# Kernel optimization log

Hardware: AMD Instinct MI355X
Metric: run time of the kernel (lower is better)

## Reference

```python
import jax, jax.numpy as jnp
import numpy as np

D_MODEL = 1024
N_STATE = 1024


def setup_inputs() -> dict:
    key = jax.random.key(0)
    k_x, k_A, k_Bw, k_Bb, k_Cw, k_Cb = jax.random.split(key, 6)
    x = jax.random.normal(k_x, (8, 2048, D_MODEL), dtype=jnp.float32)
    log_A = jax.random.normal(k_A, (N_STATE,), dtype=jnp.float32) * 0.1 - 1.0
    # nn.Linear default init: U(-1/sqrt(fan_in), 1/sqrt(fan_in)); weight is [out, in]
    bnd_B = 1.0 / np.sqrt(D_MODEL)
    B_w = jax.random.uniform(k_Bw, (N_STATE, D_MODEL), minval=-bnd_B, maxval=bnd_B, dtype=jnp.float32)
    B_b = jax.random.uniform(k_Bb, (N_STATE,), minval=-bnd_B, maxval=bnd_B, dtype=jnp.float32)
    bnd_C = 1.0 / np.sqrt(N_STATE)
    C_w = jax.random.uniform(k_Cw, (D_MODEL, N_STATE), minval=-bnd_C, maxval=bnd_C, dtype=jnp.float32)
    C_b = jax.random.uniform(k_Cb, (D_MODEL,), minval=-bnd_C, maxval=bnd_C, dtype=jnp.float32)
    return {"x": x, "log_A": log_A, "B_w": B_w, "B_b": B_b, "C_w": C_w, "C_b": C_b}


def _ssm_scan(A, B_x):
    """Diagonal linear recurrence h_t = A * h_{t-1} + B_x_t (h_0 prior = 0).

    Implemented as a parallel associative scan over the time axis.
    A: [N], B_x: [B, T, N] -> h: [B, T, N]
    """
    a = jnp.broadcast_to(A, B_x.shape)  # [B, T, N]

    def combine(c1, c2):
        a1, b1 = c1
        a2, b2 = c2
        return (a1 * a2, a2 * b1 + b2)

    _, h = jax.lax.associative_scan(combine, (a, B_x), axis=1)
    return h


def reference(x, log_A, B_w, B_b, C_w, C_b):
    A = jax.nn.sigmoid(log_A)                                  # [N]
    B_x = jnp.einsum('btd,nd->btn', x, B_w) + B_b              # [B, T, N]
    h = _ssm_scan(A, B_x)                                      # [B, T, N]
    y = jnp.einsum('btn,dn->btd', h, C_w) + C_b                # [B, T, D]
    return y
```

## Files before the change

kernel.cpp:

```cpp
#include <hip/hip_runtime.h>
#include <hip/hip_bf16.h>
#include <cstdint>
#include <cstddef>


typedef __attribute__((ext_vector_type(8))) short short8;
typedef __attribute__((ext_vector_type(4))) float f32x4;

#define AS_GLOBAL(p) ((const __attribute__((address_space(1))) void*)(p))
#define AS_LDS(p)    ((__attribute__((address_space(3))) void*)(p))

__device__ __forceinline__ unsigned short f2bf(float f) {
    union { float f; unsigned u; } v; v.f = f;
    return (unsigned short)((v.u + 0x7FFFu + ((v.u >> 16) & 1u)) >> 16);
}
__device__ __forceinline__ float bf2f(unsigned short u) {
    union { float f; unsigned u; } v; v.u = ((unsigned)u) << 16;
    return v.f;
}

__global__ void cvt_all(const float4* __restrict__ x, const float4* __restrict__ bw,
                        const float4* __restrict__ cw, ushort4* __restrict__ xo,
                        ushort4* __restrict__ bo, ushort4* __restrict__ co) {
    const int NX = (16384 * 1024) / 4;
    const int NW = (1024 * 1024) / 4;
    int i = blockIdx.x * blockDim.x + threadIdx.x;
    int stride = gridDim.x * blockDim.x;
    for (; i < NX + 2 * NW; i += stride) {
        const float4* s; ushort4* d; int j;
        if (i < NX)           { s = x;  d = xo; j = i; }
        else if (i < NX + NW) { s = bw; d = bo; j = i - NX; }
        else                  { s = cw; d = co; j = i - NX - NW; }
        float4 v = s[j];
        d[j] = make_ushort4(f2bf(v.x), f2bf(v.y), f2bf(v.z), f2bf(v.w));
    }
}

__global__ __launch_bounds__(256, 2)
void gemm1_scan_fused(const unsigned short* __restrict__ A,
                      const unsigned short* __restrict__ B,
                      const float* __restrict__ bias,
                      const float* __restrict__ logA,
                      unsigned short* __restrict__ H,
                      int M, int N, int K)
{
    constexpr int BK = 32, SXS = 130;
    __shared__ __align__(16) unsigned short smem[20800];
    unsigned short* As = smem;
    unsigned short* Bs = smem + 5120;
    unsigned short* Sx = smem;

    const int tid  = threadIdx.x;
    const int lane = tid & 63;
    const int wave = tid >> 6;
    const int wr   = wave >> 1;
    const int wm   = wr * 64;
    const int wn   = (wave & 1) * 64;
    const int q    = lane >> 4;
    const int l16  = lane & 15;
    const int m0   = blockIdx.x * 128;
    const int n0   = blockIdx.y * 128;

    const int rsub = lane >> 2;
    const int c8   = (lane & 3) * 8;

    f32x4 acc[4][4] = {};
    f32x4 accw[4]   = {};

    for (int k0 = 0; k0 < K; k0 += BK) {
        #pragma unroll
        for (int p = 0; p < 2; ++p) {
            const int rowbase = p * 64 + wave * 16;
            int gra = m0 - 32 + rowbase + rsub; if (gra < 0) gra = 0;
            const unsigned short* ga = A + (size_t)gra * K + k0 + c8;
            const unsigned short* gb = B + (size_t)(n0 + rowbase + rsub) * K + k0 + c8;
            __builtin_amdgcn_global_load_lds(AS_GLOBAL(ga), AS_LDS(&As[rowbase * BK]), 16, 0, 0);
            __builtin_amdgcn_global_load_lds(AS_GLOBAL(gb), AS_LDS(&Bs[rowbase * BK]), 16, 0, 0);
        }
        if (tid < 128) {
            const int rowbase = 128 + wave * 16;
            const unsigned short* ga = A + (size_t)(m0 - 32 + rowbase + rsub) * K + k0 + c8;
            __builtin_amdgcn_global_load_lds(AS_GLOBAL(ga), AS_LDS(&As[rowbase * BK]), 16, 0, 0);
        }
        __syncthreads();

        short8 a[4], aw, b[4];
        #pragma unroll
        for (int i = 0; i < 4; ++i)
            a[i] = *reinterpret_cast<const short8*>(&As[(32 + wm + i * 16 + l16) * BK + q * 8]);
        aw = *reinterpret_cast<const short8*>(&As[(wr * 16 + l16) * BK + q * 8]);
        #pragma unroll
        for (int j = 0; j < 4; ++j)
            b[j] = *reinterpret_cast<const short8*>(&Bs[(wn + j * 16 + l16) * BK + q * 8]);

        #pragma unroll
        for (int i = 0; i < 4; ++i)
            #pragma unroll
            for (int j = 0; j < 4; ++j)
                acc[i][j] = __builtin_amdgcn_mfma_f32_16x16x32_bf16(a[i], b[j], acc[i][j], 0, 0, 0);
        #pragma unroll
        for (int j = 0; j < 4; ++j)
            accw[j] = __builtin_amdgcn_mfma_f32_16x16x32_bf16(aw, b[j], accw[j], 0, 0, 0);
        __syncthreads();
    }

    float bcol[4];
    #pragma unroll
    for (int j = 0; j < 4; ++j)
        bcol[j] = bias[n0 + wn + j * 16 + l16];

    #pragma unroll
    for (int j = 0; j < 4; ++j) {
        #pragma unroll
        for (int r = 0; r < 4; ++r)
            Sx[(wr * 16 + q * 4 + r) * SXS + wn + j * 16 + l16] = f2bf(accw[j][r] + bcol[j]);
        #pragma unroll
        for (int i = 0; i < 4; ++i)
            #pragma unroll
            for (int r = 0; r < 4; ++r)
                Sx[(32 + wm + i * 16 + q * 4 + r) * SXS + wn + j * 16 + l16] = f2bf(acc[i][j][r] + bcol[j]);
    }
    __syncthreads();

    const int col  = tid & 127;
    const int half = tid >> 7;
    const int n    = n0 + col;
    const float Aa = 1.0f / (1.0f + __expf(-logA[n]));
    const bool chunk0 = (blockIdx.x & 15) == 0;

    float h = 0.0f;
    const int rw = half ? 64 : 0;
    if (!(half == 0 && chunk0)) {
        #pragma unroll
        for (int r = 0; r < 32; ++r)
            h = fmaf(Aa, h, bf2f(Sx[(rw + r) * SXS + col]));
    }
    const int rs = half ? 96 : 32;
    size_t o = (size_t)(m0 + (half ? 64 : 0)) * 1024 + n;
    #pragma unroll 8
    for (int r = 0; r < 64; ++r) {
        h = fmaf(Aa, h, bf2f(Sx[(rs + r) * SXS + col]));
        H[o] = f2bf(h);
        o += 1024;
    }
}

__global__ __launch_bounds__(512, 2)
void gemm2_8ph(const unsigned short* __restrict__ A,
               const unsigned short* __restrict__ B,
               const float* __restrict__ bias,
               float* __restrict__ C,
               int M, int N, int K)
{
    constexpr int BK  = 64;
    constexpr int NKT = 16;
    __shared__ __align__(16) unsigned short As[2][256 * BK];
    __shared__ __align__(16) unsigned short Bs[2][256 * BK];

    const int tid  = threadIdx.x;
    const int lane = tid & 63;
    const int wave = tid >> 6;
    const int wm   = (wave >> 2) * 128;
    const int wn   = (wave & 3) * 64;
    const int q    = lane >> 4;
    const int l16  = lane & 15;
    const int swx  = (l16 & 7) << 4;
    const int m0   = blockIdx.x * 256;
    const int n0   = blockIdx.y * 256;

    int dOff[4], sRow[4], sCol[4];
    #pragma unroll
    for (int p = 0; p < 4; ++p) {
        const int d = tid * 16 + p * 8192;
        const int l = d ^ (((d >> 7) & 7) << 4);
        dOff[p] = d;
        sRow[p] = l >> 7;
        sCol[p] = (l & 127) >> 1;
    }

    char* ldsA = (char*)As;
    char* ldsB = (char*)Bs;

    auto stage = [&](int kt) {
        const int buf = kt & 1;
        const int k0  = kt * BK;
        #pragma unroll
        for (int p = 0; p < 4; ++p) {
            const unsigned short* ga = A + (size_t)(m0 + sRow[p]) * K + k0 + sCol[p];
            const unsigned short* gb = B + (size_t)(n0 + sRow[p]) * K + k0 + sCol[p];
            __builtin_amdgcn_global_load_lds(AS_GLOBAL(ga), AS_LDS(ldsA + buf * 32768 + dOff[p]), 16, 0, 0);
            __builtin_amdgcn_global_load_lds(AS_GLOBAL(gb), AS_LDS(ldsB + buf * 32768 + dOff[p]), 16, 0, 0);
        }
    };

    f32x4 acc[8][4] = {};

    stage(0);
    stage(1);

    #pragma unroll 1
    for (int kt = 0; kt < NKT; ++kt) {
        const int buf = kt & 1;
        if (kt + 1 < NKT) asm volatile("s_waitcnt vmcnt(8)" ::: "memory");
        else              asm volatile("s_waitcnt vmcnt(0)" ::: "memory");
        __builtin_amdgcn_s_barrier();

        short8 bfrag[4][2];
        #pragma unroll
        for (int ph = 0; ph < 4; ++ph) {
            short8 afrag[2][2];
            #pragma unroll
            for (int i2 = 0; i2 < 2; ++i2)
                #pragma unroll
                for (int ks = 0; ks < 2; ++ks) {
                    const int row = wm + (ph * 2 + i2) * 16 + l16;
                    const int lby = row * 128 + ks * 64 + q * 16;
                    afrag[i2][ks] = *reinterpret_cast<const short8*>(ldsA + buf * 32768 + (lby ^ swx));
                }
            if (ph == 0) {
                #pragma unroll
                for (int j = 0; j < 4; ++j)
                    #pragma unroll
                    for (int ks = 0; ks < 2; ++ks) {
                        const int row = wn + j * 16 + l16;
                        const int lby = row * 128 + ks * 64 + q * 16;
                        bfrag[j][ks] = *reinterpret_cast<const short8*>(ldsB + buf * 32768 + (lby ^ swx));
                    }
            }
            __builtin_amdgcn_s_barrier();
            asm volatile("s_waitcnt lgkmcnt(0)" ::: "memory");
            __builtin_amdgcn_s_setprio(1);
            #pragma unroll
            for (int ks = 0; ks < 2; ++ks)
                #pragma unroll
                for (int i2 = 0; i2 < 2; ++i2)
                    #pragma unroll
                    for (int j = 0; j < 4; ++j)
                        acc[ph * 2 + i2][j] = __builtin_amdgcn_mfma_f32_16x16x32_bf16(
                            afrag[i2][ks], bfrag[j][ks], acc[ph * 2 + i2][j], 0, 0, 0);
            __builtin_amdgcn_s_setprio(0);
            __builtin_amdgcn_s_barrier();
        }
        if (kt + 2 < NKT) stage(kt + 2);
    }

    float bcol[4];
    #pragma unroll
    for (int j = 0; j < 4; ++j)
        bcol[j] = bias[n0 + wn + j * 16 + l16];

    #pragma unroll
    for (int i = 0; i < 8; ++i) {
        const int r0 = m0 + wm + i * 16 + q * 4;
        #pragma unroll
        for (int j = 0; j < 4; ++j) {
            const int col = n0 + wn + j * 16 + l16;
            #pragma unroll
            for (int r = 0; r < 4; ++r)
                C[(size_t)(r0 + r) * N + col] = acc[i][j][r] + bcol[j];
        }
    }
}

__global__ __launch_bounds__(256)
void ssm_scan(const float* __restrict__ Bx,
              const float* __restrict__ logA,
              unsigned short* __restrict__ H)
{
    constexpr int T = 2048, NS = 1024, L = 64, W = 32;
    const int tid   = threadIdx.x;
    const int bi    = blockIdx.x;
    const int ng    = bi & 3;
    const int chunk = (bi >> 2) & 31;
    const int b     = bi >> 7;
    const int n     = ng * 256 + tid;

    const float Aa = 1.0f / (1.0f + __expf(-logA[n]));
    const int t0 = chunk * L;
    int tw = t0 - W; if (tw < 0) tw = 0;

    const size_t base = (size_t)b * T * NS + n;
    float h = 0.0f;
    for (int t = tw; t < t0; ++t)
        h = fmaf(Aa, h, Bx[base + (size_t)t * NS]);

    const float* src = Bx + base + (size_t)t0 * NS;
    unsigned short* dst = H + base + (size_t)t0 * NS;
    #pragma unroll 8
    for (int t = 0; t < L; ++t) {
        h = fmaf(Aa, h, src[(size_t)t * NS]);
        dst[(size_t)t * NS] = f2bf(h);
    }
}

extern "C" void kernel_launch(void* const* d_in, const int* in_sizes, int n_in,
                              void* d_out, int out_size, void* d_ws, size_t ws_size,
                              hipStream_t stream)
{
    const float* x    = (const float*)d_in[0];
    const float* logA = (const float*)d_in[1];
    const float* Bw   = (const float*)d_in[2];
    const float* Bb   = (const float*)d_in[3];
    const float* Cw   = (const float*)d_in[4];
    const float* Cb   = (const float*)d_in[5];
    float* out = (float*)d_out;

    const int M = 8 * 2048, N = 1024, K = 1024;

    unsigned short* xh  = (unsigned short*)d_ws;
    unsigned short* Bwb = xh + (size_t)M * K;
    unsigned short* Cwb = Bwb + (size_t)N * K;
    unsigned short* hb  = Cwb + (size_t)N * K;

    const size_t need_fused = ((size_t)M * K * 2 + (size_t)N * K * 2) * 2 + (size_t)N * K * 2;

    cvt_all<<<4096, 256, 0, stream>>>((const float4*)x, (const float4*)Bw,
                                      (const float4*)Cw, (ushort4*)xh,
                                      (ushort4*)Bwb, (ushort4*)Cwb);

    dim3 grid1(M / 128, N / 128);
    dim3 grid2(M / 256, N / 256);
    if (ws_size >= need_fused) {
        gemm1_scan_fused<<<grid1, 256, 0, stream>>>(xh, Bwb, Bb, logA, hb, M, N, K);
        gemm2_8ph<<<grid2, 512, 0, stream>>>(hb, Cwb, Cb, out, M, N, K);
    } else {
        gemm2_8ph<<<grid2, 512, 0, stream>>>(xh, Bwb, Bb, out, M, N, K);
        ssm_scan<<<1024, 256, 0, stream>>>(out, logA, xh);
        gemm2_8ph<<<grid2, 512, 0, stream>>>(xh, Cwb, Cb, out, M, N, K);
    }
}
```

Before: 235.3 us.

## Split GEMM2 LDS tiles into half-tile ring slots and interleave loads across phases

Restructures the second GEMM's LDS staging into a 4-slot ring of 128-row half tiles for A and B. The global-to-LDS loads for the next k-tiles are now issued inside the compute phases rather than after the whole k-step, and the vmcnt waits move to the last phase. This lets each half-tile slot be refilled as soon as its consumers finish, so memory traffic overlaps the MFMA work more evenly and the barrier at the top of each k-step goes away. The cost is more complex waitcnt and slot bookkeeping, with a risk of race or ordering errors.

```diff
diff --git a/kernel.cpp b/kernel.cpp
--- a/kernel.cpp
+++ b/kernel.cpp
@@ -154,78 +154,97 @@
 {
     constexpr int BK  = 64;
     constexpr int NKT = 16;
-    __shared__ __align__(16) unsigned short As[2][256 * BK];
-    __shared__ __align__(16) unsigned short Bs[2][256 * BK];
+    __shared__ __align__(16) unsigned short As[4 * 8192];
+    __shared__ __align__(16) unsigned short Bs[4 * 8192];
 
     const int tid  = threadIdx.x;
     const int lane = tid & 63;
     const int wave = tid >> 6;
-    const int wm   = (wave >> 2) * 128;
+    const int wg   = wave >> 2;
+    const int wm   = wg * 128;
     const int wn   = (wave & 3) * 64;
+    const int hB   = wn >> 7;
+    const int bR0  = wn & 127;
     const int q    = lane >> 4;
     const int l16  = lane & 15;
     const int swx  = (l16 & 7) << 4;
     const int m0   = blockIdx.x * 256;
     const int n0   = blockIdx.y * 256;
 
-    int dOff[4], sRow[4], sCol[4];
-    #pragma unroll
-    for (int p = 0; p < 4; ++p) {
+    const unsigned short* aSrc[2];
+    const unsigned short* bSrc[2];
+    int dDst[2];
+    #pragma unroll
+    for (int p = 0; p < 2; ++p) {
         const int d = tid * 16 + p * 8192;
         const int l = d ^ (((d >> 7) & 7) << 4);
-        dOff[p] = d;
-        sRow[p] = l >> 7;
-        sCol[p] = (l & 127) >> 1;
+        const int srow = l >> 7;
+        const int scol = (l & 127) >> 1;
+        aSrc[p] = A + (size_t)(m0 + srow) * K + scol;
+        bSrc[p] = B + (size_t)(n0 + srow) * K + scol;
+        dDst[p] = d;
     }
 
     char* ldsA = (char*)As;
     char* ldsB = (char*)Bs;
 
-    auto stage = [&](int kt) {
-        const int buf = kt & 1;
-        const int k0  = kt * BK;
-        #pragma unroll
-        for (int p = 0; p < 4; ++p) {
-            const unsigned short* ga = A + (size_t)(m0 + sRow[p]) * K + k0 + sCol[p];
-            const unsigned short* gb = B + (size_t)(n0 + sRow[p]) * K + k0 + sCol[p];
-            __builtin_amdgcn_global_load_lds(AS_GLOBAL(ga), AS_LDS(ldsA + buf * 32768 + dOff[p]), 16, 0, 0);
-            __builtin_amdgcn_global_load_lds(AS_GLOBAL(gb), AS_LDS(ldsB + buf * 32768 + dOff[p]), 16, 0, 0);
-        }
+    auto stageA = [&](int h, int kt) {
+        const int slot = ((2 * kt + h) & 3) << 14;
+        #pragma unroll
+        for (int p = 0; p < 2; ++p)
+            __builtin_amdgcn_global_load_lds(
+                AS_GLOBAL(aSrc[p] + (size_t)h * 128 * K + kt * 64),
+                AS_LDS(ldsA + slot + dDst[p]), 16, 0, 0);
     };
+    auto stageB = [&](int h, int kt) {
+        const int slot = ((2 * kt + h) & 3) << 14;
+        #pragma unroll
+        for (int p = 0; p < 2; ++p)
+            __builtin_amdgcn_global_load_lds(
+                AS_GLOBAL(bSrc[p] + (size_t)h * 128 * K + kt * 64),
+                AS_LDS(ldsB + slot + dDst[p]), 16, 0, 0);
+    };
 
     f32x4 acc[8][4] = {};
 
-    stage(0);
-    stage(1);
+    stageA(0, 0); stageA(1, 0); stageB(0, 0); stageB(1, 0);
+    stageA(0, 1); stageA(1, 1); stageB(0, 1); stageB(1, 1);
+    asm volatile("s_waitcnt vmcnt(8)" ::: "memory");
+    __builtin_amdgcn_s_barrier();
 
     #pragma unroll 1
     for (int kt = 0; kt < NKT; ++kt) {
-        const int buf = kt & 1;
-        if (kt + 1 < NKT) asm volatile("s_waitcnt vmcnt(8)" ::: "memory");
-        else              asm volatile("s_waitcnt vmcnt(0)" ::: "memory");
-        __builtin_amdgcn_s_barrier();
-
+        const int aSlot = ((2 * kt + wg) & 3) << 14;
+        const int bSlot = ((2 * kt + hB) & 3) << 14;
         short8 bfrag[4][2];
         #pragma unroll
-        for (int ph = 0; ph < 4; ++ph) {
+        for (int p = 0; p < 4; ++p) {
             short8 afrag[2][2];
             #pragma unroll
             for (int i2 = 0; i2 < 2; ++i2)
                 #pragma unroll
                 for (int ks = 0; ks < 2; ++ks) {
-                    const int row = wm + (ph * 2 + i2) * 16 + l16;
+                    const int row = (p * 2 + i2) * 16 + l16;
                     const int lby = row * 128 + ks * 64 + q * 16;
-                    afrag[i2][ks] = *reinterpret_cast<const short8*>(ldsA + buf * 32768 + (lby ^ swx));
+                    afrag[i2][ks] = *reinterpret_cast<const short8*>(ldsA + aSlot + (lby ^ swx));
                 }
-            if (ph == 0) {
+            if (p == 0) {
                 #pragma unroll
                 for (int j = 0; j < 4; ++j)
                     #pragma unroll
                     for (int ks = 0; ks < 2; ++ks) {
-                        const int row = wn + j * 16 + l16;
+                        const int row = bR0 + j * 16 + l16;
                         const int lby = row * 128 + ks * 64 + q * 16;
-                        bfrag[j][ks] = *reinterpret_cast<const short8*>(ldsB + buf * 32768 + (lby ^ swx));
+                        bfrag[j][ks] = *reinterpret_cast<const short8*>(ldsB + bSlot + (lby ^ swx));
                     }
+            }
+            if (p == 0) { if (kt >= 1 && kt + 1 < NKT) stageA(0, kt + 1); }
+            if (p == 1) { if (kt >= 1 && kt + 1 < NKT) stageA(1, kt + 1); }
+            if (p == 2) { if (kt + 2 < NKT) stageB(0, kt + 2); }
+            if (p == 3) {
+                if (kt + 2 < NKT) stageB(1, kt + 2);
+                if (kt < NKT - 2)       asm volatile("s_waitcnt vmcnt(4)" ::: "memory");
+                else if (kt == NKT - 2) asm volatile("s_waitcnt vmcnt(0)" ::: "memory");
             }
             __builtin_amdgcn_s_barrier();
             asm volatile("s_waitcnt lgkmcnt(0)" ::: "memory");
@@ -236,12 +255,11 @@
                 for (int i2 = 0; i2 < 2; ++i2)
                     #pragma unroll
                     for (int j = 0; j < 4; ++j)
-                        acc[ph * 2 + i2][j] = __builtin_amdgcn_mfma_f32_16x16x32_bf16(
-                            afrag[i2][ks], bfrag[j][ks], acc[ph * 2 + i2][j], 0, 0, 0);
+                        acc[p * 2 + i2][j] = __builtin_amdgcn_mfma_f32_16x16x32_bf16(
+                            afrag[i2][ks], bfrag[j][ks], acc[p * 2 + i2][j], 0, 0, 0);
             __builtin_amdgcn_s_setprio(0);
             __builtin_amdgcn_s_barrier();
         }
-        if (kt + 2 < NKT) stage(kt + 2);
     }
 
     float bcol[4];
```

Result: faster. 226.3 us (-3.8%).
